# Kernel optimization log

Measured on AMD Instinct MI355X. Metric: run time of the kernel, lower is better.

The kernel has to match this reference:

```python
import jax, jax.numpy as jnp
import numpy as np

S, N, H, O = 128, 2048, 128, 128  # seq_len(=input_size), num_samples, hidden_size, output_size


def setup_inputs() -> dict:
    key = jax.random.key(0)
    ks = jax.random.split(key, 7)
    scale = 1.0 / np.sqrt(H)
    u = lambda k, shp: jax.random.uniform(k, shp, jnp.float32, -scale, scale)
    return {
        "x": jax.random.normal(ks[0], (S, N, H), jnp.float32),
        "W_ih": u(ks[1], (4 * H, H)),   # PyTorch gate order: i, f, g, o
        "W_hh": u(ks[2], (4 * H, H)),
        "b_ih": u(ks[3], (4 * H,)),
        "b_hh": u(ks[4], (4 * H,)),
        "W_out": u(ks[5], (O, H)),
        "b_out": u(ks[6], (O,)),
    }


def _lstm_forward(x, W_ih, W_hh, b_ih, b_hh, W_out, b_out):
    n, h = x.shape[1], W_hh.shape[1]
    # Precompute input contribution to gates for all timesteps: [S, N, 4H]
    xg = jnp.einsum("snh,gh->sng", x, W_ih) + (b_ih + b_hh)

    def step(carry, xt):
        h_t, c_t = carry
        gates = xt + h_t @ W_hh.T  # [N, 4H]
        i, f, g, o = jnp.split(gates, 4, axis=-1)
        i = jax.nn.sigmoid(i)
        f = jax.nn.sigmoid(f)
        g = jnp.tanh(g)
        o = jax.nn.sigmoid(o)
        c_t = f * c_t + i * g
        h_t = o * jnp.tanh(c_t)
        return (h_t, c_t), h_t

    h0 = jnp.zeros((n, h), x.dtype)  # init_hidden(): zeros
    c0 = jnp.zeros((n, h), x.dtype)
    _, out = jax.lax.scan(step, (h0, c0), xg)  # out: [S, N, H]
    # Linear projection fused over all timesteps
    pred = jnp.einsum("snh,oh->sno", out, W_out) + b_out  # [S, N, O]
    return pred


def reference(x, W_ih, W_hh, b_ih, b_hh, W_out, b_out):
    return _lstm_forward(x, W_ih, W_hh, b_ih, b_hh, W_out, b_out)
```

## Files before the change

### kernel.cpp

```cpp
#include <hip/hip_runtime.h>
#include <hip/hip_bf16.h>


#define S_LEN   128
#define N_BATCH 2048
#define H_DIM   128
#define O_DIM   128

using short8  = __attribute__((ext_vector_type(8))) short;
using short4v = __attribute__((ext_vector_type(4))) short;
using floatx4 = __attribute__((ext_vector_type(4))) float;
typedef unsigned short u16;

#define ROWP     264
#define BUFELEMS (16 * ROWP)

__device__ __forceinline__ u16 f2b(float f) {
    unsigned int u = __float_as_uint(f);
    return (u16)((u + 0x7FFF + ((u >> 16) & 1)) >> 16);
}
__device__ __forceinline__ short8 pack8(const float* p) {
    short8 r;
#pragma unroll
    for (int i = 0; i < 8; ++i) r[i] = (short)f2b(p[i]);
    return r;
}
__device__ __forceinline__ short4v pack4(float4 f) {
    short4v r;
    r[0] = (short)f2b(f.x); r[1] = (short)f2b(f.y);
    r[2] = (short)f2b(f.z); r[3] = (short)f2b(f.w);
    return r;
}
__device__ __forceinline__ float sigmoidf_fast(float v) {
    return __builtin_amdgcn_rcpf(1.0f + __builtin_amdgcn_exp2f(-1.4426950408889634f * v));
}
__device__ __forceinline__ float tanhf_fast(float v) {
    return 1.0f - 2.0f * __builtin_amdgcn_rcpf(1.0f + __builtin_amdgcn_exp2f(2.8853900817779268f * v));
}

__global__ __launch_bounds__(512, 2)
void lstm_persist(const float* __restrict__ x,
                  const float* __restrict__ W_ih,
                  const float* __restrict__ W_hh,
                  const float* __restrict__ b_ih,
                  const float* __restrict__ b_hh,
                  const float* __restrict__ W_out,
                  const float* __restrict__ b_out,
                  float* __restrict__ pred) {
    __shared__ short sh[2 * BUFELEMS];

    const int tid  = (int)threadIdx.x;
    const int wave = tid >> 6;
    const int lane = tid & 63;
    const int quad = lane >> 4;
    const int l15  = lane & 15;
    const int n0   = (int)blockIdx.x * 16;

    short8 wx[4][4], wh[4][4], wo[4];
    float  biasv[4];
#pragma unroll
    for (int t = 0; t < 4; ++t) {
        const int g = t * 128 + wave * 16 + l15;
#pragma unroll
        for (int kk = 0; kk < 4; ++kk) {
            wx[t][kk] = pack8(W_ih + g * H_DIM + kk * 32 + quad * 8);
            wh[t][kk] = pack8(W_hh + g * H_DIM + kk * 32 + quad * 8);
        }
        biasv[t] = b_ih[g] + b_hh[g];
    }
    const int ocol = wave * 16 + l15;
#pragma unroll
    for (int kk = 0; kk < 4; ++kk)
        wo[kk] = pack8(W_out + ocol * H_DIM + kk * 32 + quad * 8);
    const float bo = b_out[ocol];

    const int xm = tid >> 5;
    const int xq = (tid & 31) * 4;

    for (int i = tid; i < 16 * 128; i += 512)
        sh[(i >> 7) * ROWP + 128 + (i & 127)] = 0;
    {
        float4 f0 = *reinterpret_cast<const float4*>(x + ((size_t)(n0 + xm)) * H_DIM + xq);
        float4 f1 = *reinterpret_cast<const float4*>(x + ((size_t)N_BATCH + n0 + xm) * H_DIM + xq);
        *reinterpret_cast<short4v*>(&sh[BUFELEMS + xm * ROWP + xq]) = pack4(f0);
        *reinterpret_cast<short4v*>(&sh[xm * ROWP + xq]) = pack4(f1);
    }
    float4 xcur = *reinterpret_cast<const float4*>(x + ((size_t)2 * N_BATCH + n0 + xm) * H_DIM + xq);
    float4 xnext = *reinterpret_cast<const float4*>(x + ((size_t)3 * N_BATCH + n0 + xm) * H_DIM + xq);
    __syncthreads();

    const int arow = l15 * ROWP + quad * 8;
    const int hcol = 128 + wave * 16 + l15;

    floatx4 xg0 = {biasv[0], biasv[0], biasv[0], biasv[0]};
    floatx4 xg1 = {biasv[1], biasv[1], biasv[1], biasv[1]};
    floatx4 xg2 = {biasv[2], biasv[2], biasv[2], biasv[2]};
    floatx4 xg3 = {biasv[3], biasv[3], biasv[3], biasv[3]};
#pragma unroll
    for (int kk = 0; kk < 4; ++kk) {
        short8 a = *reinterpret_cast<const short8*>(&sh[BUFELEMS + arow + kk * 32]);
        xg0 = __builtin_amdgcn_mfma_f32_16x16x32_bf16(a, wx[0][kk], xg0, 0, 0, 0);
        xg1 = __builtin_amdgcn_mfma_f32_16x16x32_bf16(a, wx[1][kk], xg1, 0, 0, 0);
        xg2 = __builtin_amdgcn_mfma_f32_16x16x32_bf16(a, wx[2][kk], xg2, 0, 0, 0);
        xg3 = __builtin_amdgcn_mfma_f32_16x16x32_bf16(a, wx[3][kk], xg3, 0, 0, 0);
    }
    __syncthreads();

    float cc[4] = {0.f, 0.f, 0.f, 0.f};

    for (int s = 0; s < S_LEN; ++s) {
        short* shb = sh + (s & 1) * BUFELEMS;
        short* shn = sh + ((s & 1) ^ 1) * BUFELEMS;

        floatx4 g0 = xg0, g1 = xg1, g2 = xg2, g3 = xg3;
        floatx4 ao = {bo, bo, bo, bo};

#pragma unroll
        for (int kk = 0; kk < 4; ++kk) {
            short8 ah = *reinterpret_cast<const short8*>(&shb[arow + 128 + kk * 32]);
            g0 = __builtin_amdgcn_mfma_f32_16x16x32_bf16(ah, wh[0][kk], g0, 0, 0, 0);
            g1 = __builtin_amdgcn_mfma_f32_16x16x32_bf16(ah, wh[1][kk], g1, 0, 0, 0);
            g2 = __builtin_amdgcn_mfma_f32_16x16x32_bf16(ah, wh[2][kk], g2, 0, 0, 0);
            g3 = __builtin_amdgcn_mfma_f32_16x16x32_bf16(ah, wh[3][kk], g3, 0, 0, 0);
            ao = __builtin_amdgcn_mfma_f32_16x16x32_bf16(ah, wo[kk], ao, 0, 0, 0);
        }

        if (s > 0) {
            size_t base = ((size_t)(s - 1) * N_BATCH + n0 + quad * 4) * O_DIM + wave * 16 + l15;
#pragma unroll
            for (int r = 0; r < 4; ++r)
                pred[base + (size_t)r * O_DIM] = ao[r];
        }

        xg0 = floatx4{biasv[0], biasv[0], biasv[0], biasv[0]};
        xg1 = floatx4{biasv[1], biasv[1], biasv[1], biasv[1]};
        xg2 = floatx4{biasv[2], biasv[2], biasv[2], biasv[2]};
        xg3 = floatx4{biasv[3], biasv[3], biasv[3], biasv[3]};
#pragma unroll
        for (int kk = 0; kk < 4; ++kk) {
            short8 axv = *reinterpret_cast<const short8*>(&shb[arow + kk * 32]);
            xg0 = __builtin_amdgcn_mfma_f32_16x16x32_bf16(axv, wx[0][kk], xg0, 0, 0, 0);
            xg1 = __builtin_amdgcn_mfma_f32_16x16x32_bf16(axv, wx[1][kk], xg1, 0, 0, 0);
            xg2 = __builtin_amdgcn_mfma_f32_16x16x32_bf16(axv, wx[2][kk], xg2, 0, 0, 0);
            xg3 = __builtin_amdgcn_mfma_f32_16x16x32_bf16(axv, wx[3][kk], xg3, 0, 0, 0);
        }

        if (s <= 125)
            *reinterpret_cast<short4v*>(&shn[xm * ROWP + xq]) = pack4(xcur);
        if (s <= 124)
            xnext = *reinterpret_cast<const float4*>(
                x + ((size_t)(s + 3) * N_BATCH + n0 + xm) * H_DIM + xq);

        float hv[4];
#pragma unroll
        for (int r = 0; r < 4; ++r) {
            float iv = sigmoidf_fast(g0[r]);
            float fv = sigmoidf_fast(g1[r]);
            float gv = tanhf_fast(g2[r]);
            float ov = sigmoidf_fast(g3[r]);
            cc[r] = fv * cc[r] + iv * gv;
            hv[r] = ov * tanhf_fast(cc[r]);
        }
#pragma unroll
        for (int r = 0; r < 4; ++r)
            shn[(quad * 4 + r) * ROWP + hcol] = (short)f2b(hv[r]);

        xcur = xnext;
        __syncthreads();
    }

    floatx4 ao = {bo, bo, bo, bo};
#pragma unroll
    for (int kk = 0; kk < 4; ++kk) {
        short8 ah = *reinterpret_cast<const short8*>(&sh[arow + 128 + kk * 32]);
        ao = __builtin_amdgcn_mfma_f32_16x16x32_bf16(ah, wo[kk], ao, 0, 0, 0);
    }
    size_t base = ((size_t)(S_LEN - 1) * N_BATCH + n0 + quad * 4) * O_DIM + wave * 16 + l15;
#pragma unroll
    for (int r = 0; r < 4; ++r)
        pred[base + (size_t)r * O_DIM] = ao[r];
}

extern "C" void kernel_launch(void* const* d_in, const int* in_sizes, int n_in,
                              void* d_out, int out_size, void* d_ws, size_t ws_size,
                              hipStream_t stream) {
    const float* x    = (const float*)d_in[0];
    const float* Wih  = (const float*)d_in[1];
    const float* Whh  = (const float*)d_in[2];
    const float* bih  = (const float*)d_in[3];
    const float* bhh  = (const float*)d_in[4];
    const float* Wout = (const float*)d_in[5];
    const float* bout = (const float*)d_in[6];
    float* pred = (float*)d_out;

    lstm_persist<<<dim3(N_BATCH / 16), dim3(512), 0, stream>>>(
        x, Wih, Whh, bih, bhh, Wout, bout, pred);
}
```

Before: 359.9 us.

## Transpose MFMA operands, split gate accumulators, vectorize h and pred stores

```diff
diff --git a/kernel.cpp b/kernel.cpp
--- a/kernel.cpp
+++ b/kernel.cpp
@@ -14,6 +14,8 @@
 
 #define ROWP     264
 #define BUFELEMS (16 * ROWP)
+
+#define BAR() asm volatile("s_waitcnt lgkmcnt(0)\n\ts_barrier" ::: "memory")
 
 __device__ __forceinline__ u16 f2b(float f) {
     unsigned int u = __float_as_uint(f);
@@ -55,9 +57,10 @@
     const int quad = lane >> 4;
     const int l15  = lane & 15;
     const int n0   = (int)blockIdx.x * 16;
+    const int jrow = wave * 16 + quad * 4;
 
     short8 wx[4][4], wh[4][4], wo[4];
-    float  biasv[4];
+    floatx4 biasv[4];
 #pragma unroll
     for (int t = 0; t < 4; ++t) {
         const int g = t * 128 + wave * 16 + l15;
@@ -66,13 +69,14 @@
             wx[t][kk] = pack8(W_ih + g * H_DIM + kk * 32 + quad * 8);
             wh[t][kk] = pack8(W_hh + g * H_DIM + kk * 32 + quad * 8);
         }
-        biasv[t] = b_ih[g] + b_hh[g];
-    }
-    const int ocol = wave * 16 + l15;
+        float4 bi = *reinterpret_cast<const float4*>(b_ih + t * 128 + jrow);
+        float4 bh = *reinterpret_cast<const float4*>(b_hh + t * 128 + jrow);
+        biasv[t] = floatx4{bi.x + bh.x, bi.y + bh.y, bi.z + bh.z, bi.w + bh.w};
+    }
 #pragma unroll
     for (int kk = 0; kk < 4; ++kk)
-        wo[kk] = pack8(W_out + ocol * H_DIM + kk * 32 + quad * 8);
-    const float bo = b_out[ocol];
+        wo[kk] = pack8(W_out + (wave * 16 + l15) * H_DIM + kk * 32 + quad * 8);
+    float4 bo4 = *reinterpret_cast<const float4*>(b_out + jrow);
 
     const int xm = tid >> 5;
     const int xq = (tid & 31) * 4;
@@ -85,26 +89,22 @@
         *reinterpret_cast<short4v*>(&sh[BUFELEMS + xm * ROWP + xq]) = pack4(f0);
         *reinterpret_cast<short4v*>(&sh[xm * ROWP + xq]) = pack4(f1);
     }
-    float4 xcur = *reinterpret_cast<const float4*>(x + ((size_t)2 * N_BATCH + n0 + xm) * H_DIM + xq);
+    float4 xcur  = *reinterpret_cast<const float4*>(x + ((size_t)2 * N_BATCH + n0 + xm) * H_DIM + xq);
     float4 xnext = *reinterpret_cast<const float4*>(x + ((size_t)3 * N_BATCH + n0 + xm) * H_DIM + xq);
-    __syncthreads();
+    BAR();
 
     const int arow = l15 * ROWP + quad * 8;
-    const int hcol = 128 + wave * 16 + l15;
-
-    floatx4 xg0 = {biasv[0], biasv[0], biasv[0], biasv[0]};
-    floatx4 xg1 = {biasv[1], biasv[1], biasv[1], biasv[1]};
-    floatx4 xg2 = {biasv[2], biasv[2], biasv[2], biasv[2]};
-    floatx4 xg3 = {biasv[3], biasv[3], biasv[3], biasv[3]};
+
+    floatx4 xg0 = biasv[0], xg1 = biasv[1], xg2 = biasv[2], xg3 = biasv[3];
 #pragma unroll
     for (int kk = 0; kk < 4; ++kk) {
-        short8 a = *reinterpret_cast<const short8*>(&sh[BUFELEMS + arow + kk * 32]);
-        xg0 = __builtin_amdgcn_mfma_f32_16x16x32_bf16(a, wx[0][kk], xg0, 0, 0, 0);
-        xg1 = __builtin_amdgcn_mfma_f32_16x16x32_bf16(a, wx[1][kk], xg1, 0, 0, 0);
-        xg2 = __builtin_amdgcn_mfma_f32_16x16x32_bf16(a, wx[2][kk], xg2, 0, 0, 0);
-        xg3 = __builtin_amdgcn_mfma_f32_16x16x32_bf16(a, wx[3][kk], xg3, 0, 0, 0);
-    }
-    __syncthreads();
+        short8 ax = *reinterpret_cast<const short8*>(&sh[BUFELEMS + arow + kk * 32]);
+        xg0 = __builtin_amdgcn_mfma_f32_16x16x32_bf16(wx[0][kk], ax, xg0, 0, 0, 0);
+        xg1 = __builtin_amdgcn_mfma_f32_16x16x32_bf16(wx[1][kk], ax, xg1, 0, 0, 0);
+        xg2 = __builtin_amdgcn_mfma_f32_16x16x32_bf16(wx[2][kk], ax, xg2, 0, 0, 0);
+        xg3 = __builtin_amdgcn_mfma_f32_16x16x32_bf16(wx[3][kk], ax, xg3, 0, 0, 0);
+    }
+    BAR();
 
     float cc[4] = {0.f, 0.f, 0.f, 0.f};
 
@@ -112,37 +112,50 @@
         short* shb = sh + (s & 1) * BUFELEMS;
         short* shn = sh + ((s & 1) ^ 1) * BUFELEMS;
 
-        floatx4 g0 = xg0, g1 = xg1, g2 = xg2, g3 = xg3;
-        floatx4 ao = {bo, bo, bo, bo};
-
+        short8 ah0 = *reinterpret_cast<const short8*>(&shb[arow + 128 + 0 * 32]);
+        short8 ah1 = *reinterpret_cast<const short8*>(&shb[arow + 128 + 1 * 32]);
+        short8 ah2 = *reinterpret_cast<const short8*>(&shb[arow + 128 + 2 * 32]);
+        short8 ah3 = *reinterpret_cast<const short8*>(&shb[arow + 128 + 3 * 32]);
+
+        floatx4 g0a = xg0, g1a = xg1, g2a = xg2, g3a = xg3;
+        floatx4 g0b = {0,0,0,0}, g1b = {0,0,0,0}, g2b = {0,0,0,0}, g3b = {0,0,0,0};
+        floatx4 ao = {bo4.x, bo4.y, bo4.z, bo4.w};
+
+        g0a = __builtin_amdgcn_mfma_f32_16x16x32_bf16(wh[0][0], ah0, g0a, 0, 0, 0);
+        g1a = __builtin_amdgcn_mfma_f32_16x16x32_bf16(wh[1][0], ah0, g1a, 0, 0, 0);
+        g2a = __builtin_amdgcn_mfma_f32_16x16x32_bf16(wh[2][0], ah0, g2a, 0, 0, 0);
+        g3a = __builtin_amdgcn_mfma_f32_16x16x32_bf16(wh[3][0], ah0, g3a, 0, 0, 0);
+        g0b = __builtin_amdgcn_mfma_f32_16x16x32_bf16(wh[0][1], ah1, g0b, 0, 0, 0);
+        g1b = __builtin_amdgcn_mfma_f32_16x16x32_bf16(wh[1][1], ah1, g1b, 0, 0, 0);
+        g2b = __builtin_amdgcn_mfma_f32_16x16x32_bf16(wh[2][1], ah1, g2b, 0, 0, 0);
+        g3b = __builtin_amdgcn_mfma_f32_16x16x32_bf16(wh[3][1], ah1, g3b, 0, 0, 0);
+        ao  = __builtin_amdgcn_mfma_f32_16x16x32_bf16(wo[0],    ah0, ao,  0, 0, 0);
+        g0a = __builtin_amdgcn_mfma_f32_16x16x32_bf16(wh[0][2], ah2, g0a, 0, 0, 0);
+        g1a = __builtin_amdgcn_mfma_f32_16x16x32_bf16(wh[1][2], ah2, g1a, 0, 0, 0);
+        g2a = __builtin_amdgcn_mfma_f32_16x16x32_bf16(wh[2][2], ah2, g2a, 0, 0, 0);
+        g3a = __builtin_amdgcn_mfma_f32_16x16x32_bf16(wh[3][2], ah2, g3a, 0, 0, 0);
+        ao  = __builtin_amdgcn_mfma_f32_16x16x32_bf16(wo[1],    ah1, ao,  0, 0, 0);
+        g0b = __builtin_amdgcn_mfma_f32_16x16x32_bf16(wh[0][3], ah3, g0b, 0, 0, 0);
+        g1b = __builtin_amdgcn_mfma_f32_16x16x32_bf16(wh[1][3], ah3, g1b, 0, 0, 0);
+        g2b = __builtin_amdgcn_mfma_f32_16x16x32_bf16(wh[2][3], ah3, g2b, 0, 0, 0);
+        g3b = __builtin_amdgcn_mfma_f32_16x16x32_bf16(wh[3][3], ah3, g3b, 0, 0, 0);
+        ao  = __builtin_amdgcn_mfma_f32_16x16x32_bf16(wo[2],    ah2, ao,  0, 0, 0);
+        ao  = __builtin_amdgcn_mfma_f32_16x16x32_bf16(wo[3],    ah3, ao,  0, 0, 0);
+
+        xg0 = biasv[0]; xg1 = biasv[1]; xg2 = biasv[2]; xg3 = biasv[3];
 #pragma unroll
         for (int kk = 0; kk < 4; ++kk) {
-            short8 ah = *reinterpret_cast<const short8*>(&shb[arow + 128 + kk * 32]);
-            g0 = __builtin_amdgcn_mfma_f32_16x16x32_bf16(ah, wh[0][kk], g0, 0, 0, 0);
-            g1 = __builtin_amdgcn_mfma_f32_16x16x32_bf16(ah, wh[1][kk], g1, 0, 0, 0);
-            g2 = __builtin_amdgcn_mfma_f32_16x16x32_bf16(ah, wh[2][kk], g2, 0, 0, 0);
-            g3 = __builtin_amdgcn_mfma_f32_16x16x32_bf16(ah, wh[3][kk], g3, 0, 0, 0);
-            ao = __builtin_amdgcn_mfma_f32_16x16x32_bf16(ah, wo[kk], ao, 0, 0, 0);
+            short8 ax = *reinterpret_cast<const short8*>(&shb[arow + kk * 32]);
+            xg0 = __builtin_amdgcn_mfma_f32_16x16x32_bf16(wx[0][kk], ax, xg0, 0, 0, 0);
+            xg1 = __builtin_amdgcn_mfma_f32_16x16x32_bf16(wx[1][kk], ax, xg1, 0, 0, 0);
+            xg2 = __builtin_amdgcn_mfma_f32_16x16x32_bf16(wx[2][kk], ax, xg2, 0, 0, 0);
+            xg3 = __builtin_amdgcn_mfma_f32_16x16x32_bf16(wx[3][kk], ax, xg3, 0, 0, 0);
         }
 
         if (s > 0) {
-            size_t base = ((size_t)(s - 1) * N_BATCH + n0 + quad * 4) * O_DIM + wave * 16 + l15;
-#pragma unroll
-            for (int r = 0; r < 4; ++r)
-                pred[base + (size_t)r * O_DIM] = ao[r];
-        }
-
-        xg0 = floatx4{biasv[0], biasv[0], biasv[0], biasv[0]};
-        xg1 = floatx4{biasv[1], biasv[1], biasv[1], biasv[1]};
-        xg2 = floatx4{biasv[2], biasv[2], biasv[2], biasv[2]};
-        xg3 = floatx4{biasv[3], biasv[3], biasv[3], biasv[3]};
-#pragma unroll
-        for (int kk = 0; kk < 4; ++kk) {
-            short8 axv = *reinterpret_cast<const short8*>(&shb[arow + kk * 32]);
-            xg0 = __builtin_amdgcn_mfma_f32_16x16x32_bf16(axv, wx[0][kk], xg0, 0, 0, 0);
-            xg1 = __builtin_amdgcn_mfma_f32_16x16x32_bf16(axv, wx[1][kk], xg1, 0, 0, 0);
-            xg2 = __builtin_amdgcn_mfma_f32_16x16x32_bf16(axv, wx[2][kk], xg2, 0, 0, 0);
-            xg3 = __builtin_amdgcn_mfma_f32_16x16x32_bf16(axv, wx[3][kk], xg3, 0, 0, 0);
+            float4 po = {ao[0], ao[1], ao[2], ao[3]};
+            *reinterpret_cast<float4*>(
+                pred + ((size_t)(s - 1) * N_BATCH + n0 + l15) * O_DIM + jrow) = po;
         }
 
         if (s <= 125)
@@ -151,34 +164,31 @@
             xnext = *reinterpret_cast<const float4*>(
                 x + ((size_t)(s + 3) * N_BATCH + n0 + xm) * H_DIM + xq);
 
-        float hv[4];
+        short4v hp;
 #pragma unroll
         for (int r = 0; r < 4; ++r) {
-            float iv = sigmoidf_fast(g0[r]);
-            float fv = sigmoidf_fast(g1[r]);
-            float gv = tanhf_fast(g2[r]);
-            float ov = sigmoidf_fast(g3[r]);
+            float iv = sigmoidf_fast(g0a[r] + g0b[r]);
+            float fv = sigmoidf_fast(g1a[r] + g1b[r]);
+            float gv = tanhf_fast(g2a[r] + g2b[r]);
+            float ov = sigmoidf_fast(g3a[r] + g3b[r]);
             cc[r] = fv * cc[r] + iv * gv;
-            hv[r] = ov * tanhf_fast(cc[r]);
-        }
-#pragma unroll
-        for (int r = 0; r < 4; ++r)
-            shn[(quad * 4 + r) * ROWP + hcol] = (short)f2b(hv[r]);
+            hp[r] = (short)f2b(ov * tanhf_fast(cc[r]));
+        }
+        *reinterpret_cast<short4v*>(&shn[l15 * ROWP + 128 + jrow]) = hp;
 
         xcur = xnext;
-        __syncthreads();
-    }
-
-    floatx4 ao = {bo, bo, bo, bo};
+        BAR();
+    }
+
+    floatx4 ao = {bo4.x, bo4.y, bo4.z, bo4.w};
 #pragma unroll
     for (int kk = 0; kk < 4; ++kk) {
         short8 ah = *reinterpret_cast<const short8*>(&sh[arow + 128 + kk * 32]);
-        ao = __builtin_amdgcn_mfma_f32_16x16x32_bf16(ah, wo[kk], ao, 0, 0, 0);
-    }
-    size_t base = ((size_t)(S_LEN - 1) * N_BATCH + n0 + quad * 4) * O_DIM + wave * 16 + l15;
-#pragma unroll
-    for (int r = 0; r < 4; ++r)
-        pred[base + (size_t)r * O_DIM] = ao[r];
+        ao = __builtin_amdgcn_mfma_f32_16x16x32_bf16(wo[kk], ah, ao, 0, 0, 0);
+    }
+    float4 po = {ao[0], ao[1], ao[2], ao[3]};
+    *reinterpret_cast<float4*>(
+        pred + ((size_t)(S_LEN - 1) * N_BATCH + n0 + l15) * O_DIM + jrow) = po;
 }
 
 extern "C" void kernel_launch(void* const* d_in, const int* in_sizes, int n_in,
```

New measurement: 360.8 us. About the same (+0.2%).
